# Kernel tuning notes

Measured on AMD Instinct MI355X. Metric: run time of the kernel, lower is better.

## Reference

```python
import jax, jax.numpy as jnp
import numpy as np

N_NODES = 20000
N_EDGES = 200000
N_GRAPHS = 128
IN_DIM = 256
HID = 512
HEADS = 8
C = HID // HEADS  # 64
LAT = 256
NEG_SLOPE = 0.2
BN_EPS = 1e-5


def setup_inputs() -> dict:
    key = jax.random.key(0)
    ks = jax.random.split(key, 24)
    n = lambda k, s, sc=0.05: jax.random.normal(k, s, jnp.float32) * sc
    return {
        'x': jax.random.normal(ks[0], (N_NODES, IN_DIM), jnp.float32),
        'edge_index': jax.random.randint(ks[1], (2, N_EDGES), 0, N_NODES, jnp.int32),
        'batch': jnp.sort(jax.random.randint(ks[2], (N_NODES,), 0, N_GRAPHS, jnp.int32)),
        'Wl0': n(ks[3], (IN_DIM, HID)), 'bl0': n(ks[4], (HID,)),
        'Wr0': n(ks[5], (IN_DIM, HID)), 'br0': n(ks[6], (HID,)),
        'att0': n(ks[7], (HEADS, C)), 'bias0': n(ks[8], (HID,)),
        'Wl1': n(ks[9], (HID, HID)), 'bl1': n(ks[10], (HID,)),
        'Wr1': n(ks[11], (HID, HID)), 'br1': n(ks[12], (HID,)),
        'att1': n(ks[13], (HEADS, C)), 'bias1': n(ks[14], (HID,)),
        'bn_gamma': jnp.ones((HID,), jnp.float32),
        'bn_beta': jnp.zeros((HID,), jnp.float32),
        'bn_mean': n(ks[15], (HID,)),
        'bn_var': jax.random.uniform(ks[16], (HID,), jnp.float32, 0.5, 1.5),
        'Wfc': n(ks[17], (HID, LAT)), 'bfc': n(ks[18], (LAT,)),
    }


def gatv2_layer(x, src, dst, Wl, bl, Wr, br, att, bias):
    # x: [N, F]; returns [N, HEADS*C]. GATv2: e = a . LeakyReLU(Wl x_src + Wr x_dst)
    xl = (x @ Wl + bl).reshape(-1, HEADS, C)  # source transform [N,H,C]
    xr = (x @ Wr + br).reshape(-1, HEADS, C)  # target transform [N,H,C]
    feat = jax.nn.leaky_relu(xl[src] + xr[dst], NEG_SLOPE)     # [E,H,C]
    logits = jnp.einsum('ehc,hc->eh', feat, att)               # [E,H]
    # segment softmax over incoming edges of each target node
    m = jax.ops.segment_max(logits, dst, num_segments=N_NODES)  # [N,H]
    p = jnp.exp(logits - m[dst])
    denom = jax.ops.segment_sum(p, dst, num_segments=N_NODES)   # [N,H]
    alpha = p / (denom[dst] + 1e-16)                            # [E,H]
    msg = xl[src] * alpha[:, :, None]                           # [E,H,C]
    out = jax.ops.segment_sum(msg, dst, num_segments=N_NODES)   # [N,H,C]
    return out.reshape(-1, HEADS * C) + bias


def reference(x, edge_index, batch, Wl0, bl0, Wr0, br0, att0, bias0,
              Wl1, bl1, Wr1, br1, att1, bias1,
              bn_gamma, bn_beta, bn_mean, bn_var, Wfc, bfc):
    src, dst = edge_index[0], edge_index[1]
    # layer 0 + ELU (dropout is identity in eval mode)
    h = jax.nn.elu(gatv2_layer(x, src, dst, Wl0, bl0, Wr0, br0, att0, bias0))
    # layer 1 + ELU
    h = jax.nn.elu(gatv2_layer(h, src, dst, Wl1, bl1, Wr1, br1, att1, bias1))
    # global add pool over graphs
    g = jax.ops.segment_sum(h, batch, num_segments=N_GRAPHS)  # [G, HID]
    # BatchNorm1d (eval mode: running stats)
    g = (g - bn_mean) * jax.lax.rsqrt(bn_var + BN_EPS) * bn_gamma + bn_beta
    return g @ Wfc + bfc  # [G, LAT]
```

## Files before the change

kernel.cpp:

```cpp
#include <hip/hip_runtime.h>
#include <hip/hip_bf16.h>
#include <cstdint>

#define NN 20000
#define NE 200000
#define NG 128
#define HID 512
#define XLR_W 1024

typedef __attribute__((ext_vector_type(4))) float f32x4;
typedef __attribute__((ext_vector_type(8))) short s16x8;

__device__ __forceinline__ float bf2f(unsigned short u) {
  union { unsigned int i; float f; } v; v.i = ((unsigned int)u) << 16; return v.f;
}
__device__ __forceinline__ unsigned short f2bf(float f) {
  union { float f; unsigned int i; } v; v.f = f;
  unsigned int i = v.i + 0x7FFFu + ((v.i >> 16) & 1u);
  return (unsigned short)(i >> 16);
}
__device__ __forceinline__ float asf(unsigned int u) {
  union { unsigned int i; float f; } v; v.i = u; return v.f;
}

#define GLOAD16(gp, lp)                                                        \
  __builtin_amdgcn_global_load_lds(                                            \
      (const __attribute__((address_space(1))) unsigned int*)(gp),             \
      (__attribute__((address_space(3))) unsigned int*)(lp), 16, 0, 0)

__global__ void k_cast(const float* __restrict__ in, unsigned short* __restrict__ out, int n4) {
  int i = blockIdx.x * blockDim.x + threadIdx.x;
  if (i < n4) {
    float4 v = ((const float4*)in)[i];
    ushort4 o;
    o.x = f2bf(v.x); o.y = f2bf(v.y); o.z = f2bf(v.z); o.w = f2bf(v.w);
    ((ushort4*)out)[i] = o;
  }
}

__global__ void k_hist(const int* __restrict__ dst, int* __restrict__ deg, int E) {
  int i = blockIdx.x * blockDim.x + threadIdx.x;
  if (i < E) atomicAdd(&deg[dst[i]], 1);
}

__global__ __launch_bounds__(1024) void k_scan1(const int* __restrict__ deg,
                                                int* __restrict__ offs,
                                                int* __restrict__ btot, int n) {
  __shared__ int wsum[16];
  int t = threadIdx.x;
  int wid = t >> 6, lane = t & 63;
  int i = blockIdx.x * 1024 + t;
  int v = (i < n) ? deg[i] : 0;
  int s = v;
#pragma unroll
  for (int off = 1; off < 64; off <<= 1) {
    int x = __shfl_up(s, off, 64);
    if (lane >= off) s += x;
  }
  if (lane == 63) wsum[wid] = s;
  __syncthreads();
  if (wid == 0) {
    int ws = (lane < 16) ? wsum[lane] : 0;
#pragma unroll
    for (int off = 1; off < 16; off <<= 1) {
      int x = __shfl_up(ws, off, 64);
      if (lane >= off) ws += x;
    }
    if (lane < 16) wsum[lane] = ws;
  }
  __syncthreads();
  int ex = s - v + (wid ? wsum[wid - 1] : 0);
  if (i < n) offs[i] = ex;
  if (t == 1023) btot[blockIdx.x] = ex + v;
}

__global__ void k_scan2(const int* __restrict__ btot, int* __restrict__ bofs,
                        int nb, int* __restrict__ offs, int n) {
  int lane = threadIdx.x;
  int v = (lane < nb) ? btot[lane] : 0;
  int s = v;
#pragma unroll
  for (int off = 1; off < 32; off <<= 1) {
    int x = __shfl_up(s, off, 64);
    if (lane >= off) s += x;
  }
  if (lane < nb) bofs[lane] = s - v;
  if (lane == nb - 1) offs[n] = s;
}

__global__ __launch_bounds__(1024) void k_scan3(int* __restrict__ offs,
                                                const int* __restrict__ bofs,
                                                int* __restrict__ woff, int n) {
  int i = blockIdx.x * 1024 + threadIdx.x;
  if (i < n) {
    int v = offs[i] + bofs[blockIdx.x];
    offs[i] = v;
    woff[i] = v;
  }
}

__global__ void k_scatter(const int* __restrict__ src, const int* __restrict__ dst,
                          int* __restrict__ woff, int* __restrict__ src_s, int E) {
  int i = blockIdx.x * blockDim.x + threadIdx.x;
  if (i < E) {
    int d = dst[i];
    int pos = atomicAdd(&woff[d], 1);
    src_s[pos] = src[i];
  }
}

__global__ void k_pack(const float* __restrict__ Wl, const float* __restrict__ bl,
                       const float* __restrict__ Wr, const float* __restrict__ br,
                       unsigned short* __restrict__ wt, float* __restrict__ bcat, int kshift) {
  int id = blockIdx.x * blockDim.x + threadIdx.x;
  int K = 1 << kshift;
  int total = XLR_W << kshift;
  if (id < total) {
    int nrow = id >> kshift, k = id & (K - 1);
    float v = (nrow < HID) ? Wl[k * HID + nrow] : Wr[k * HID + (nrow - HID)];
    wt[id] = f2bf(v);
  }
  if (id < XLR_W) bcat[id] = (id < HID) ? bl[id] : br[id - HID];
}

#define BM 128
#define BN 128
#define BK 32

__global__ __launch_bounds__(256) void k_gemm(const unsigned short* __restrict__ A,
                                              const unsigned short* __restrict__ Bt,
                                              const float* __restrict__ bias,
                                              unsigned short* __restrict__ C,
                                              int M, int N, int K) {
  __shared__ __align__(16) unsigned short As[BM * BK];
  __shared__ __align__(16) unsigned short Bs[BN * BK];
  int m0 = blockIdx.y * BM, n0 = blockIdx.x * BN;
  int t = threadIdx.x;
  int wave = t >> 6, lane = t & 63;
  int wm = (wave >> 1) * 64, wn = (wave & 1) * 64;
  int ml = lane & 15, mq = lane >> 4;
  int lr = lane >> 2;
  int lc = (lane & 3) * 8;

  f32x4 acc[4][4];
#pragma unroll
  for (int i = 0; i < 4; i++)
#pragma unroll
    for (int j = 0; j < 4; j++) acc[i][j] = (f32x4)0.0f;

  int ar0 = m0 + wave * 32 + lr;      if (ar0 > M - 1) ar0 = M - 1;
  int ar1 = m0 + wave * 32 + 16 + lr; if (ar1 > M - 1) ar1 = M - 1;
  const unsigned short* ga0 = A + (size_t)ar0 * K + lc;
  const unsigned short* ga1 = A + (size_t)ar1 * K + lc;
  const unsigned short* gb0 = Bt + (size_t)(n0 + wave * 32 + lr) * K + lc;
  const unsigned short* gb1 = gb0 + (size_t)16 * K;
  unsigned short* la0 = &As[(wave * 32) * BK];
  unsigned short* la1 = &As[(wave * 32 + 16) * BK];
  unsigned short* lb0 = &Bs[(wave * 32) * BK];
  unsigned short* lb1 = &Bs[(wave * 32 + 16) * BK];

  for (int k0 = 0; k0 < K; k0 += BK) {
    GLOAD16(ga0, la0);
    GLOAD16(ga1, la1);
    GLOAD16(gb0, lb0);
    GLOAD16(gb1, lb1);
    ga0 += BK; ga1 += BK; gb0 += BK; gb1 += BK;
    __syncthreads();
    s16x8 af[4], bfr[4];
#pragma unroll
    for (int i = 0; i < 4; i++)
      af[i] = *(const s16x8*)(&As[(wm + i * 16 + ml) * BK + mq * 8]);
#pragma unroll
    for (int j = 0; j < 4; j++)
      bfr[j] = *(const s16x8*)(&Bs[(wn + j * 16 + ml) * BK + mq * 8]);
#pragma unroll
    for (int i = 0; i < 4; i++)
#pragma unroll
      for (int j = 0; j < 4; j++)
        acc[i][j] = __builtin_amdgcn_mfma_f32_16x16x32_bf16(af[i], bfr[j], acc[i][j], 0, 0, 0);
    __syncthreads();
  }

#pragma unroll
  for (int i = 0; i < 4; i++) {
#pragma unroll
    for (int j = 0; j < 4; j++) {
      int col = n0 + wn + j * 16 + ml;
      float bcol = bias[col];
#pragma unroll
      for (int r = 0; r < 4; r++) {
        int row = m0 + wm + i * 16 + mq * 4 + r;
        if (row < M) C[(size_t)row * N + col] = f2bf(acc[i][j][r] + bcol);
      }
    }
  }
}

__global__ __launch_bounds__(256) void k_attn(const unsigned short* __restrict__ xlr,
                                              const float* __restrict__ att,
                                              const int* __restrict__ offs,
                                              const int* __restrict__ src_s,
                                              const float* __restrict__ bias,
                                              unsigned short* __restrict__ hout) {
  __shared__ float red[4][8][68];
  __shared__ float reds[4][8];
  int n = blockIdx.x;
  int wave = threadIdx.x >> 6, lane = threadIdx.x & 63;
  int h = lane >> 3, k = lane & 7;
  int c = h * 64 + k * 8;
  int s0 = offs[n], s1 = offs[n + 1];

  uint4 uxr = *(const uint4*)(xlr + (size_t)n * XLR_W + HID + c);
  float xr[8];
  xr[0] = asf(uxr.x << 16); xr[1] = asf(uxr.x & 0xFFFF0000u);
  xr[2] = asf(uxr.y << 16); xr[3] = asf(uxr.y & 0xFFFF0000u);
  xr[4] = asf(uxr.z << 16); xr[5] = asf(uxr.z & 0xFFFF0000u);
  xr[6] = asf(uxr.w << 16); xr[7] = asf(uxr.w & 0xFFFF0000u);
  float at[8];
  {
    const float4* ap = (const float4*)(att + c);
    float4 a0 = ap[0], a1 = ap[1];
    at[0] = a0.x; at[1] = a0.y; at[2] = a0.z; at[3] = a0.w;
    at[4] = a1.x; at[5] = a1.y; at[6] = a1.z; at[7] = a1.w;
  }

  float acc[8] = {0.f, 0.f, 0.f, 0.f, 0.f, 0.f, 0.f, 0.f};
  float sum = 0.0f;

  int i = s0 + wave;
  uint4 u_cur = make_uint4(0, 0, 0, 0);
  if (i < s1) {
    int s = src_s[i];
    u_cur = *(const uint4*)(xlr + (size_t)s * XLR_W + c);
  }
  int nx = i + 4;
  for (; i < s1; i += 4) {
    uint4 u = u_cur;
    if (nx < s1) {
      int s = src_s[nx];
      u_cur = *(const uint4*)(xlr + (size_t)s * XLR_W + c);
    }
    nx += 4;

    float xl[8];
    xl[0] = asf(u.x << 16); xl[1] = asf(u.x & 0xFFFF0000u);
    xl[2] = asf(u.y << 16); xl[3] = asf(u.y & 0xFFFF0000u);
    xl[4] = asf(u.z << 16); xl[5] = asf(u.z & 0xFFFF0000u);
    xl[6] = asf(u.w << 16); xl[7] = asf(u.w & 0xFFFF0000u);

    float l = 0.0f;
#pragma unroll
    for (int j = 0; j < 8; j++) {
      float v = xl[j] + xr[j];
      v = fmaf(0.4f, fabsf(v), 0.6f * v);
      l = fmaf(v, at[j], l);
    }
    l += __shfl_xor(l, 1, 64);
    l += __shfl_xor(l, 2, 64);
    l += __shfl_xor(l, 4, 64);

    float p = __expf(l);
    sum += p;
#pragma unroll
    for (int j = 0; j < 8; j++) acc[j] = fmaf(p, xl[j], acc[j]);
  }

#pragma unroll
  for (int j = 0; j < 8; j++) red[wave][h][k * 8 + j] = acc[j];
  if (k == 0) reds[wave][h] = sum;
  __syncthreads();

  int t = threadIdx.x;
  int cc = t * 2;
  int hh = cc >> 6, off = cc & 63;
  float a0 = red[0][hh][off] + red[1][hh][off] + red[2][hh][off] + red[3][hh][off];
  float a1 = red[0][hh][off + 1] + red[1][hh][off + 1] + red[2][hh][off + 1] + red[3][hh][off + 1];
  float sm = reds[0][hh] + reds[1][hh] + reds[2][hh] + reds[3][hh];
  float di = 1.0f / (sm + 1e-16f);
  float o_a = a0 * di + bias[cc];
  float o_b = a1 * di + bias[cc + 1];
  o_a = o_a > 0.0f ? o_a : (__expf(o_a) - 1.0f);
  o_b = o_b > 0.0f ? o_b : (__expf(o_b) - 1.0f);
  unsigned int up = (unsigned int)f2bf(o_a) | ((unsigned int)f2bf(o_b) << 16);
  *(unsigned int*)(hout + (size_t)n * HID + cc) = up;
}

__device__ __forceinline__ int lower_bound(const int* __restrict__ a, int n, int key) {
  int lo = 0, hi = n;
  while (lo < hi) { int mid = (lo + hi) >> 1; if (a[mid] < key) lo = mid + 1; else hi = mid; }
  return lo;
}

__global__ __launch_bounds__(256) void k_pool(const unsigned short* __restrict__ h,
                                              const int* __restrict__ batch,
                                              float* __restrict__ part) {
  int g = blockIdx.x, p = blockIdx.y, t = threadIdx.x;
  int start = lower_bound(batch, NN, g);
  int end = lower_bound(batch, NN, g + 1);
  int cntq = (end - start + 3) >> 2;
  int lo = start + p * cntq;
  int hi = lo + cntq; if (hi > end) hi = end;
  int c = t * 2;
  float a0 = 0.0f, a1 = 0.0f;
  for (int n = lo; n < hi; n++) {
    unsigned int u = *(const unsigned int*)(h + (size_t)n * HID + c);
    a0 += asf(u << 16);
    a1 += asf(u & 0xFFFF0000u);
  }
  float* dstp = part + ((size_t)g * 4 + p) * HID + c;
  dstp[0] = a0;
  dstp[1] = a1;
}

__global__ __launch_bounds__(256) void k_fc(const float* __restrict__ part,
                                            const float* __restrict__ gamma,
                                            const float* __restrict__ beta,
                                            const float* __restrict__ mean,
                                            const float* __restrict__ var,
                                            const float* __restrict__ Wfc,
                                            const float* __restrict__ bfc,
                                            float* __restrict__ out) {
  __shared__ float xsm[512];
  int g = blockIdx.x, t = threadIdx.x;
  for (int c = t; c < HID; c += 256) {
    float s = part[((size_t)g * 4 + 0) * HID + c] + part[((size_t)g * 4 + 1) * HID + c]
            + part[((size_t)g * 4 + 2) * HID + c] + part[((size_t)g * 4 + 3) * HID + c];
    xsm[c] = (s - mean[c]) * rsqrtf(var[c] + 1e-5f) * gamma[c] + beta[c];
  }
  __syncthreads();
  float acc = bfc[t];
#pragma unroll 8
  for (int k = 0; k < 512; k++) acc += xsm[k] * Wfc[k * 256 + t];
  out[g * 256 + t] = acc;
}

extern "C" void kernel_launch(void* const* d_in, const int* in_sizes, int n_in,
                              void* d_out, int out_size, void* d_ws, size_t ws_size,
                              hipStream_t stream) {
  const float* x     = (const float*)d_in[0];
  const int* ei      = (const int*)d_in[1];
  const int* batch   = (const int*)d_in[2];
  const float* Wl0   = (const float*)d_in[3];
  const float* bl0   = (const float*)d_in[4];
  const float* Wr0   = (const float*)d_in[5];
  const float* br0   = (const float*)d_in[6];
  const float* att0  = (const float*)d_in[7];
  const float* bias0 = (const float*)d_in[8];
  const float* Wl1   = (const float*)d_in[9];
  const float* bl1   = (const float*)d_in[10];
  const float* Wr1   = (const float*)d_in[11];
  const float* br1   = (const float*)d_in[12];
  const float* att1  = (const float*)d_in[13];
  const float* bias1 = (const float*)d_in[14];
  const float* gamma = (const float*)d_in[15];
  const float* beta  = (const float*)d_in[16];
  const float* mean  = (const float*)d_in[17];
  const float* var   = (const float*)d_in[18];
  const float* Wfc   = (const float*)d_in[19];
  const float* bfc   = (const float*)d_in[20];

  const int* src = ei;
  const int* dst = ei + NE;

  char* w = (char*)d_ws;
  size_t off = 0;
  auto alloc = [&](size_t bytes) -> void* {
    void* p = w + off;
    off += (bytes + 255) & ~(size_t)255;
    return p;
  };
  int* deg            = (int*)alloc((size_t)NN * 4);
  int* offs           = (int*)alloc((size_t)(NN + 1) * 4);
  int* woff           = (int*)alloc((size_t)NN * 4);
  int* src_s          = (int*)alloc((size_t)NE * 4);
  int* btot           = (int*)alloc((size_t)32 * 4);
  int* bofs           = (int*)alloc((size_t)32 * 4);
  unsigned short* xb  = (unsigned short*)alloc((size_t)NN * 256 * 2);
  unsigned short* xlr = (unsigned short*)alloc((size_t)NN * XLR_W * 2);
  unsigned short* hb  = (unsigned short*)alloc((size_t)NN * HID * 2);
  unsigned short* wt  = (unsigned short*)alloc((size_t)XLR_W * HID * 2);
  float* bcat         = (float*)alloc((size_t)XLR_W * 4);
  float* part         = (float*)alloc((size_t)NG * 4 * HID * 4);

  const int NB = (NN + 1023) / 1024;

  hipMemsetAsync(deg, 0, (size_t)NN * 4, stream);
  k_hist<<<(NE + 255) / 256, 256, 0, stream>>>(dst, deg, NE);
  k_scan1<<<NB, 1024, 0, stream>>>(deg, offs, btot, NN);
  k_scan2<<<1, 64, 0, stream>>>(btot, bofs, NB, offs, NN);
  k_scan3<<<NB, 1024, 0, stream>>>(offs, bofs, woff, NN);
  k_scatter<<<(NE + 255) / 256, 256, 0, stream>>>(src, dst, woff, src_s, NE);

  k_cast<<<(NN * 256 / 4 + 255) / 256, 256, 0, stream>>>(x, xb, NN * 256 / 4);

  k_pack<<<(XLR_W * 256 + 255) / 256, 256, 0, stream>>>(Wl0, bl0, Wr0, br0, wt, bcat, 8);
  k_gemm<<<dim3(XLR_W / BN, (NN + BM - 1) / BM), 256, 0, stream>>>(xb, wt, bcat, xlr, NN, XLR_W, 256);
  k_attn<<<NN, 256, 0, stream>>>(xlr, att0, offs, src_s, bias0, hb);

  k_pack<<<(XLR_W * 512 + 255) / 256, 256, 0, stream>>>(Wl1, bl1, Wr1, br1, wt, bcat, 9);
  k_gemm<<<dim3(XLR_W / BN, (NN + BM - 1) / BM), 256, 0, stream>>>(hb, wt, bcat, xlr, NN, XLR_W, 512);
  k_attn<<<NN, 256, 0, stream>>>(xlr, att1, offs, src_s, bias1, hb);

  k_pool<<<dim3(NG, 4), 256, 0, stream>>>(hb, batch, part);
  k_fc<<<NG, 256, 0, stream>>>(part, gamma, beta, mean, var, Wfc, bfc, (float*)d_out);
}
```

Measured before the change: 336.9 us.

## Fuse prep kernels, merge scan stages, double-buffer GEMM LDS tiles

```diff
diff --git a/kernel.cpp b/kernel.cpp
--- a/kernel.cpp
+++ b/kernel.cpp
@@ -28,13 +28,37 @@
       (const __attribute__((address_space(1))) unsigned int*)(gp),             \
       (__attribute__((address_space(3))) unsigned int*)(lp), 16, 0, 0)
 
-__global__ void k_cast(const float* __restrict__ in, unsigned short* __restrict__ out, int n4) {
-  int i = blockIdx.x * blockDim.x + threadIdx.x;
-  if (i < n4) {
-    float4 v = ((const float4*)in)[i];
+__global__ __launch_bounds__(256) void k_prep(const float* __restrict__ x,
+                                              unsigned short* __restrict__ xb,
+                                              const float* __restrict__ Wl0, const float* __restrict__ bl0,
+                                              const float* __restrict__ Wr0, const float* __restrict__ br0,
+                                              unsigned short* __restrict__ wt0, float* __restrict__ bcat0,
+                                              const float* __restrict__ Wl1, const float* __restrict__ bl1,
+                                              const float* __restrict__ Wr1, const float* __restrict__ br1,
+                                              unsigned short* __restrict__ wt1, float* __restrict__ bcat1,
+                                              int* __restrict__ deg) {
+  int b = blockIdx.x, t = threadIdx.x;
+  if (b < 79) {
+    int i = b * 256 + t;
+    if (i < NN) deg[i] = 0;
+  } else if (b < 5079) {
+    int i = (b - 79) * 256 + t;
+    float4 v = ((const float4*)x)[i];
     ushort4 o;
     o.x = f2bf(v.x); o.y = f2bf(v.y); o.z = f2bf(v.z); o.w = f2bf(v.w);
-    ((ushort4*)out)[i] = o;
+    ((ushort4*)xb)[i] = o;
+  } else if (b < 6103) {
+    int id = (b - 5079) * 256 + t;
+    int nrow = id >> 8, k = id & 255;
+    float v = (nrow < HID) ? Wl0[k * HID + nrow] : Wr0[k * HID + (nrow - HID)];
+    wt0[id] = f2bf(v);
+    if (id < XLR_W) bcat0[id] = (id < HID) ? bl0[id] : br0[id - HID];
+  } else {
+    int id = (b - 6103) * 256 + t;
+    int nrow = id >> 9, k = id & 511;
+    float v = (nrow < HID) ? Wl1[k * HID + nrow] : Wr1[k * HID + (nrow - HID)];
+    wt1[id] = f2bf(v);
+    if (id < XLR_W) bcat1[id] = (id < HID) ? bl1[id] : br1[id - HID];
   }
 }
 
@@ -74,26 +98,27 @@
   if (t == 1023) btot[blockIdx.x] = ex + v;
 }
 
-__global__ void k_scan2(const int* __restrict__ btot, int* __restrict__ bofs,
-                        int nb, int* __restrict__ offs, int n) {
-  int lane = threadIdx.x;
-  int v = (lane < nb) ? btot[lane] : 0;
-  int s = v;
-#pragma unroll
-  for (int off = 1; off < 32; off <<= 1) {
-    int x = __shfl_up(s, off, 64);
-    if (lane >= off) s += x;
-  }
-  if (lane < nb) bofs[lane] = s - v;
-  if (lane == nb - 1) offs[n] = s;
-}
-
 __global__ __launch_bounds__(1024) void k_scan3(int* __restrict__ offs,
-                                                const int* __restrict__ bofs,
-                                                int* __restrict__ woff, int n) {
-  int i = blockIdx.x * 1024 + threadIdx.x;
+                                                const int* __restrict__ btot,
+                                                int* __restrict__ woff, int n, int nb) {
+  __shared__ int sbofs;
+  int t = threadIdx.x;
+  if (t < 64) {
+    int v = (t < nb) ? btot[t] : 0;
+    int s = v;
+#pragma unroll
+    for (int off = 1; off < 64; off <<= 1) {
+      int x = __shfl_up(s, off, 64);
+      if (t >= off) s += x;
+    }
+    if (t == (int)blockIdx.x) sbofs = s - v;
+    if (blockIdx.x == (unsigned)(nb - 1) && t == nb - 1) offs[n] = s;
+  }
+  __syncthreads();
+  int add = sbofs;
+  int i = blockIdx.x * 1024 + t;
   if (i < n) {
-    int v = offs[i] + bofs[blockIdx.x];
+    int v = offs[i] + add;
     offs[i] = v;
     woff[i] = v;
   }
@@ -109,20 +134,6 @@
   }
 }
 
-__global__ void k_pack(const float* __restrict__ Wl, const float* __restrict__ bl,
-                       const float* __restrict__ Wr, const float* __restrict__ br,
-                       unsigned short* __restrict__ wt, float* __restrict__ bcat, int kshift) {
-  int id = blockIdx.x * blockDim.x + threadIdx.x;
-  int K = 1 << kshift;
-  int total = XLR_W << kshift;
-  if (id < total) {
-    int nrow = id >> kshift, k = id & (K - 1);
-    float v = (nrow < HID) ? Wl[k * HID + nrow] : Wr[k * HID + (nrow - HID)];
-    wt[id] = f2bf(v);
-  }
-  if (id < XLR_W) bcat[id] = (id < HID) ? bl[id] : br[id - HID];
-}
-
 #define BM 128
 #define BN 128
 #define BK 32
@@ -132,8 +143,8 @@
                                               const float* __restrict__ bias,
                                               unsigned short* __restrict__ C,
                                               int M, int N, int K) {
-  __shared__ __align__(16) unsigned short As[BM * BK];
-  __shared__ __align__(16) unsigned short Bs[BN * BK];
+  __shared__ __align__(16) unsigned short As[2][BM * BK];
+  __shared__ __align__(16) unsigned short Bs[2][BN * BK];
   int m0 = blockIdx.y * BM, n0 = blockIdx.x * BN;
   int t = threadIdx.x;
   int wave = t >> 6, lane = t & 63;
@@ -154,31 +165,38 @@
   const unsigned short* ga1 = A + (size_t)ar1 * K + lc;
   const unsigned short* gb0 = Bt + (size_t)(n0 + wave * 32 + lr) * K + lc;
   const unsigned short* gb1 = gb0 + (size_t)16 * K;
-  unsigned short* la0 = &As[(wave * 32) * BK];
-  unsigned short* la1 = &As[(wave * 32 + 16) * BK];
-  unsigned short* lb0 = &Bs[(wave * 32) * BK];
-  unsigned short* lb1 = &Bs[(wave * 32 + 16) * BK];
-
-  for (int k0 = 0; k0 < K; k0 += BK) {
-    GLOAD16(ga0, la0);
-    GLOAD16(ga1, la1);
-    GLOAD16(gb0, lb0);
-    GLOAD16(gb1, lb1);
-    ga0 += BK; ga1 += BK; gb0 += BK; gb1 += BK;
+  int lo0 = (wave * 32) * BK;
+  int lo1 = (wave * 32 + 16) * BK;
+
+  GLOAD16(ga0, &As[0][lo0]);
+  GLOAD16(ga1, &As[0][lo1]);
+  GLOAD16(gb0, &Bs[0][lo0]);
+  GLOAD16(gb1, &Bs[0][lo1]);
+  ga0 += BK; ga1 += BK; gb0 += BK; gb1 += BK;
+
+  int T = K / BK;
+  for (int tt = 0; tt < T; tt++) {
+    int cur = tt & 1, nxt = cur ^ 1;
     __syncthreads();
+    if (tt + 1 < T) {
+      GLOAD16(ga0, &As[nxt][lo0]);
+      GLOAD16(ga1, &As[nxt][lo1]);
+      GLOAD16(gb0, &Bs[nxt][lo0]);
+      GLOAD16(gb1, &Bs[nxt][lo1]);
+      ga0 += BK; ga1 += BK; gb0 += BK; gb1 += BK;
+    }
     s16x8 af[4], bfr[4];
 #pragma unroll
     for (int i = 0; i < 4; i++)
-      af[i] = *(const s16x8*)(&As[(wm + i * 16 + ml) * BK + mq * 8]);
+      af[i] = *(const s16x8*)(&As[cur][(wm + i * 16 + ml) * BK + mq * 8]);
 #pragma unroll
     for (int j = 0; j < 4; j++)
-      bfr[j] = *(const s16x8*)(&Bs[(wn + j * 16 + ml) * BK + mq * 8]);
+      bfr[j] = *(const s16x8*)(&Bs[cur][(wn + j * 16 + ml) * BK + mq * 8]);
 #pragma unroll
     for (int i = 0; i < 4; i++)
 #pragma unroll
       for (int j = 0; j < 4; j++)
         acc[i][j] = __builtin_amdgcn_mfma_f32_16x16x32_bf16(af[i], bfr[j], acc[i][j], 0, 0, 0);
-    __syncthreads();
   }
 
 #pragma unroll
@@ -374,31 +392,28 @@
   int* woff           = (int*)alloc((size_t)NN * 4);
   int* src_s          = (int*)alloc((size_t)NE * 4);
   int* btot           = (int*)alloc((size_t)32 * 4);
-  int* bofs           = (int*)alloc((size_t)32 * 4);
   unsigned short* xb  = (unsigned short*)alloc((size_t)NN * 256 * 2);
   unsigned short* xlr = (unsigned short*)alloc((size_t)NN * XLR_W * 2);
   unsigned short* hb  = (unsigned short*)alloc((size_t)NN * HID * 2);
-  unsigned short* wt  = (unsigned short*)alloc((size_t)XLR_W * HID * 2);
-  float* bcat         = (float*)alloc((size_t)XLR_W * 4);
+  unsigned short* wt0 = (unsigned short*)alloc((size_t)XLR_W * 256 * 2);
+  unsigned short* wt1 = (unsigned short*)alloc((size_t)XLR_W * HID * 2);
+  float* bcat0        = (float*)alloc((size_t)XLR_W * 4);
+  float* bcat1        = (float*)alloc((size_t)XLR_W * 4);
   float* part         = (float*)alloc((size_t)NG * 4 * HID * 4);
 
   const int NB = (NN + 1023) / 1024;
 
-  hipMemsetAsync(deg, 0, (size_t)NN * 4, stream);
+  k_prep<<<8151, 256, 0, stream>>>(x, xb, Wl0, bl0, Wr0, br0, wt0, bcat0,
+                                   Wl1, bl1, Wr1, br1, wt1, bcat1, deg);
   k_hist<<<(NE + 255) / 256, 256, 0, stream>>>(dst, deg, NE);
   k_scan1<<<NB, 1024, 0, stream>>>(deg, offs, btot, NN);
-  k_scan2<<<1, 64, 0, stream>>>(btot, bofs, NB, offs, NN);
-  k_scan3<<<NB, 1024, 0, stream>>>(offs, bofs, woff, NN);
+  k_scan3<<<NB, 1024, 0, stream>>>(offs, btot, woff, NN, NB);
   k_scatter<<<(NE + 255) / 256, 256, 0, stream>>>(src, dst, woff, src_s, NE);
 
-  k_cast<<<(NN * 256 / 4 + 255) / 256, 256, 0, stream>>>(x, xb, NN * 256 / 4);
-
-  k_pack<<<(XLR_W * 256 + 255) / 256, 256, 0, stream>>>(Wl0, bl0, Wr0, br0, wt, bcat, 8);
-  k_gemm<<<dim3(XLR_W / BN, (NN + BM - 1) / BM), 256, 0, stream>>>(xb, wt, bcat, xlr, NN, XLR_W, 256);
+  k_gemm<<<dim3(XLR_W / BN, (NN + BM - 1) / BM), 256, 0, stream>>>(xb, wt0, bcat0, xlr, NN, XLR_W, 256);
   k_attn<<<NN, 256, 0, stream>>>(xlr, att0, offs, src_s, bias0, hb);
 
-  k_pack<<<(XLR_W * 512 + 255) / 256, 256, 0, stream>>>(Wl1, bl1, Wr1, br1, wt, bcat, 9);
-  k_gemm<<<dim3(XLR_W / BN, (NN + BM - 1) / BM), 256, 0, stream>>>(hb, wt, bcat, xlr, NN, XLR_W, 512);
+  k_gemm<<<dim3(XLR_W / BN, (NN + BM - 1) / BM), 256, 0, stream>>>(hb, wt1, bcat1, xlr, NN, XLR_W, 512);
   k_attn<<<NN, 256, 0, stream>>>(xlr, att1, offs, src_s, bias1, hb);
 
   k_pool<<<dim3(NG, 4), 256, 0, stream>>>(hb, batch, part);
```

Result: no change. 340.5 us (+1.1%).
